# Kernel tuning notes

Hardware: AMD Instinct MI355X
Metric: run time of the kernel (lower is better)

## Reference

```python
import jax, jax.numpy as jnp
import numpy as np

N = 100000      # number of edge features (rows of feats)
M = 800000      # number of triplets
HID = 128
HEADS = 8
DH = HID // HEADS


def setup_inputs() -> dict:
    key = jax.random.key(0)
    ks = jax.random.split(key, 10)
    s = 1.0 / np.sqrt(HID)
    inp = {
        "feats": jax.random.normal(ks[0], (N, HID), dtype=jnp.float32),
        "idx_kj": jax.random.randint(ks[1], (M,), 0, N, dtype=jnp.int64),
        "idx_ji": jax.random.randint(ks[2], (M,), 0, N, dtype=jnp.int64),
        "Wv": jax.random.uniform(ks[3], (HID, HID), jnp.float32, -s, s),
        "Wq": jax.random.uniform(ks[4], (HID, HID), jnp.float32, -s, s),
        "Wk": jax.random.uniform(ks[5], (HID, HID), jnp.float32, -s, s),
        "W1": jax.random.uniform(ks[6], (HID, HID), jnp.float32, -s, s),
        "b1": jax.random.uniform(ks[7], (HID,), jnp.float32, -s, s),
        "W2": jax.random.uniform(ks[8], (HID, HID), jnp.float32, -s, s),
        "b2": jax.random.uniform(ks[9], (HID,), jnp.float32, -s, s),
    }
    return inp


def reference(feats, idx_kj, idx_ji, Wv, Wq, Wk, W1, b1, W2, b2):
    # Projections (no bias), reshape to [N, H, Dh]
    v = (feats @ Wv.T).reshape(N, HEADS, DH)
    k = (feats @ Wk.T).reshape(N, HEADS, DH)
    q = (feats @ Wq.T).reshape(N, HEADS, DH)

    # edge-indexed attention scores: [M, H, 1]
    att = jnp.sum(q[idx_kj] * k[idx_ji], axis=-1, keepdims=True)
    att = jnp.exp(jax.nn.leaky_relu(att, negative_slope=0.2))  # unsafe softmax, as in source

    # segment-sum normalizer over destination index idx_ji: [N, H, 1]
    denom = jax.ops.segment_sum(att, idx_ji, num_segments=N)
    att = att / denom[idx_ji]

    # weighted V gather-scatter: [M, HID] -> [N, HID]
    v_att = (v[idx_kj] * att).reshape(M, HID)
    agg = jax.ops.segment_sum(v_att, idx_ji, num_segments=N)  # v_clone after +scatter-v

    v_flat = v.reshape(N, HID)
    # ResidualLayer (dropout in eval mode -> identity): v + relu(lin2(relu(lin1(agg))))
    h = jax.nn.relu(agg @ W1.T + b1)
    h = jax.nn.relu(h @ W2.T + b2)
    return v_flat + h
```

## Files before the change

kernel.cpp:

```cpp
#include <hip/hip_runtime.h>
#include <hip/hip_bf16.h>
#include <math.h>

#define N_NODES 100000
#define M_EDGES 800000
#define HID 128
#define HEADS 8
#define DH 16
#define SCAN_NB ((N_NODES + 1023) / 1024)

typedef __attribute__((ext_vector_type(8))) short short8;
typedef __attribute__((ext_vector_type(4))) float floatx4;

__device__ __forceinline__ ushort f32_to_bf16(float x) {
    __hip_bfloat16 h = __float2bfloat16(x);
    union { __hip_bfloat16 h; ushort u; } c; c.h = h;
    return c.u;
}
__device__ __forceinline__ float bf16_bits_to_f32(ushort u) {
    union { unsigned int i; float f; } c; c.i = ((unsigned int)u) << 16;
    return c.f;
}
__device__ __forceinline__ float bf16pair_lo(unsigned int p) {
    union { unsigned int i; float f; } c; c.i = p << 16; return c.f;
}
__device__ __forceinline__ float bf16pair_hi(unsigned int p) {
    union { unsigned int i; float f; } c; c.i = p & 0xffff0000u; return c.f;
}

__device__ __forceinline__ void stage_w_frag(const ushort* __restrict__ W,
                                             ushort* __restrict__ lds, int tid)
{
    #pragma unroll
    for (int i = 0; i < 8; ++i) {
        int idx  = i * 256 + tid;
        int f    = idx >> 6;
        int lane = idx & 63;
        int t    = f & 7, ks = f >> 3;
        int row  = t * 16 + (lane & 15);
        int col  = ks * 32 + (lane >> 4) * 8;
        uint4 d = *(const uint4*)(W + row * HID + col);
        *(uint4*)(lds + idx * 8) = d;
    }
}

__global__ __launch_bounds__(256) void cvt_w_kernel(
    const float* __restrict__ Wq, const float* __restrict__ Wk, const float* __restrict__ Wv,
    const float* __restrict__ W1, const float* __restrict__ W2,
    ushort* __restrict__ dq, ushort* __restrict__ dk, ushort* __restrict__ dv,
    ushort* __restrict__ d1, ushort* __restrict__ d2)
{
    int i = blockIdx.x * 256 + threadIdx.x;
    int w = i >> 14;
    int j = i & 16383;
    const float* s[5] = {Wq, Wk, Wv, W1, W2};
    ushort*      d[5] = {dq, dk, dv, d1, d2};
    d[w][j] = f32_to_bf16(s[w][j]);
}

__global__ __launch_bounds__(256) void qkv_mfma_kernel(
    const float* __restrict__ feats,
    const ushort* __restrict__ Wq16, const ushort* __restrict__ Wk16, const ushort* __restrict__ Wv16,
    ushort* __restrict__ q16, ushort* __restrict__ k16, ushort* __restrict__ v16)
{
    __shared__ ushort wlds[16384];
    const int tid  = threadIdx.x;
    const int wave = tid >> 6;
    const int lane = tid & 63;
    const int row0 = blockIdx.x * 128 + wave * 32;
    const int lrow = lane & 15;
    const int lk   = (lane >> 4) * 8;
    const int crow = (lane >> 4) * 4;

    short8 afrag[2][4];
    bool tvalid[2];
    #pragma unroll
    for (int r = 0; r < 2; ++r) {
        int rr = row0 + r * 16;
        tvalid[r] = (rr < N_NODES);
        const float* arow = feats + (size_t)((tvalid[r] ? rr : 0) + lrow) * HID + lk;
        #pragma unroll
        for (int ks = 0; ks < 4; ++ks) {
            float4 f0 = *(const float4*)(arow + ks * 32);
            float4 f1 = *(const float4*)(arow + ks * 32 + 4);
            short8 a;
            a[0] = (short)f32_to_bf16(f0.x); a[1] = (short)f32_to_bf16(f0.y);
            a[2] = (short)f32_to_bf16(f0.z); a[3] = (short)f32_to_bf16(f0.w);
            a[4] = (short)f32_to_bf16(f1.x); a[5] = (short)f32_to_bf16(f1.y);
            a[6] = (short)f32_to_bf16(f1.z); a[7] = (short)f32_to_bf16(f1.w);
            afrag[r][ks] = a;
        }
    }

    const ushort* Ws[3] = {Wq16, Wk16, Wv16};
    ushort*       Os[3] = {q16, k16, v16};

    #pragma unroll
    for (int w = 0; w < 3; ++w) {
        __syncthreads();
        stage_w_frag(Ws[w], wlds, tid);
        __syncthreads();

        floatx4 acc[2][8];
        #pragma unroll
        for (int r = 0; r < 2; ++r)
            #pragma unroll
            for (int t = 0; t < 8; ++t) acc[r][t] = (floatx4)(0.f);

        #pragma unroll
        for (int ks = 0; ks < 4; ++ks) {
            short8 B[8];
            #pragma unroll
            for (int t = 0; t < 8; ++t)
                B[t] = *(const short8*)&wlds[(ks * 8 + t) * 512 + lane * 8];
            #pragma unroll
            for (int t = 0; t < 8; ++t) {
                acc[0][t] = __builtin_amdgcn_mfma_f32_16x16x32_bf16(B[t], afrag[0][ks], acc[0][t], 0, 0, 0);
                acc[1][t] = __builtin_amdgcn_mfma_f32_16x16x32_bf16(B[t], afrag[1][ks], acc[1][t], 0, 0, 0);
            }
        }

        #pragma unroll
        for (int r = 0; r < 2; ++r) {
            if (tvalid[r]) {
                ushort* O = Os[w] + (size_t)(row0 + r * 16 + lrow) * HID;
                #pragma unroll
                for (int t = 0; t < 8; ++t) {
                    ushort4 o;
                    o.x = f32_to_bf16(acc[r][t][0]); o.y = f32_to_bf16(acc[r][t][1]);
                    o.z = f32_to_bf16(acc[r][t][2]); o.w = f32_to_bf16(acc[r][t][3]);
                    *(ushort4*)(O + t * 16 + crow) = o;
                }
            }
        }
    }
}

__global__ __launch_bounds__(256) void hist_kernel(
    const int* __restrict__ idx_ji, int* __restrict__ count)
{
    int m = blockIdx.x * 256 + threadIdx.x;
    if (m < M_EDGES) atomicAdd(&count[idx_ji[m]], 1);
}

__global__ __launch_bounds__(256) void scan_blocksum_kernel(
    const int* __restrict__ count, int* __restrict__ blocksum)
{
    __shared__ int s[256];
    const int tid = threadIdx.x;
    const int base = blockIdx.x * 1024 + tid * 4;
    int sum = 0;
    if (base + 3 < N_NODES) {
        int4 c = *(const int4*)(count + base);
        sum = c.x + c.y + c.z + c.w;
    } else {
        #pragma unroll
        for (int j = 0; j < 4; ++j) if (base + j < N_NODES) sum += count[base + j];
    }
    s[tid] = sum;
    __syncthreads();
    for (int off = 128; off > 0; off >>= 1) {
        if (tid < off) s[tid] += s[tid + off];
        __syncthreads();
    }
    if (tid == 0) blocksum[blockIdx.x] = s[0];
}

__global__ __launch_bounds__(128) void scan_top_kernel(int* __restrict__ blocksum)
{
    __shared__ int s[128];
    const int t = threadIdx.x;
    int v = (t < SCAN_NB) ? blocksum[t] : 0;
    s[t] = v;
    __syncthreads();
    for (int off = 1; off < 128; off <<= 1) {
        int x = (t >= off) ? s[t - off] : 0;
        __syncthreads();
        s[t] += x;
        __syncthreads();
    }
    if (t < SCAN_NB) blocksum[t] = s[t] - v;
}

__global__ __launch_bounds__(256) void scan_write_kernel(
    const int* __restrict__ count, const int* __restrict__ blocksum,
    int* __restrict__ offsets, int* __restrict__ cursor)
{
    __shared__ int s[256];
    const int tid = threadIdx.x;
    const int base = blockIdx.x * 1024 + tid * 4;
    int c0 = 0, c1 = 0, c2 = 0, c3 = 0;
    if (base + 3 < N_NODES) {
        int4 c = *(const int4*)(count + base);
        c0 = c.x; c1 = c.y; c2 = c.z; c3 = c.w;
    } else {
        if (base     < N_NODES) c0 = count[base];
        if (base + 1 < N_NODES) c1 = count[base + 1];
        if (base + 2 < N_NODES) c2 = count[base + 2];
        if (base + 3 < N_NODES) c3 = count[base + 3];
    }
    const int tsum = c0 + c1 + c2 + c3;
    s[tid] = tsum;
    __syncthreads();
    for (int off = 1; off < 256; off <<= 1) {
        int x = (tid >= off) ? s[tid - off] : 0;
        __syncthreads();
        s[tid] += x;
        __syncthreads();
    }
    int o0 = s[tid] - tsum + blocksum[blockIdx.x];
    int o1 = o0 + c0, o2 = o1 + c1, o3 = o2 + c2;
    if (base + 3 < N_NODES) {
        *(int4*)(offsets + base) = make_int4(o0, o1, o2, o3);
        *(int4*)(cursor  + base) = make_int4(o0, o1, o2, o3);
    } else {
        if (base     < N_NODES) { offsets[base]     = o0; cursor[base]     = o0; }
        if (base + 1 < N_NODES) { offsets[base + 1] = o1; cursor[base + 1] = o1; }
        if (base + 2 < N_NODES) { offsets[base + 2] = o2; cursor[base + 2] = o2; }
        if (base + 3 < N_NODES) { offsets[base + 3] = o3; cursor[base + 3] = o3; }
    }
}

__global__ __launch_bounds__(256) void fill_kernel(
    const int* __restrict__ idx_ji, const int* __restrict__ idx_kj,
    int* __restrict__ cursor, int* __restrict__ edge_kj)
{
    int m = blockIdx.x * 256 + threadIdx.x;
    if (m < M_EDGES) {
        int pos = atomicAdd(&cursor[idx_ji[m]], 1);
        edge_kj[pos] = idx_kj[m];
    }
}

__global__ __launch_bounds__(256) void aggregate_kernel(
    const int* __restrict__ edge_kj, const int* __restrict__ offsets,
    const int* __restrict__ count, const ushort* __restrict__ q16,
    const ushort* __restrict__ k16, const ushort* __restrict__ v16,
    ushort* __restrict__ agg16)
{
    int gid  = blockIdx.x * 256 + threadIdx.x;
    int node = gid >> 6;
    int lane = threadIdx.x & 63;
    if (node >= N_NODES) return;

    const int deg  = count[node];
    const int base = offsets[node];

    unsigned int knp = *(const unsigned int*)(k16 + (size_t)node * HID + lane * 2);
    const float knx = bf16pair_lo(knp), kny = bf16pair_hi(knp);
    float accx = 0.f, accy = 0.f, d = 0.f;

    int e = 0;
    for (; e + 4 <= deg; e += 4) {
        int kj[4];
        #pragma unroll
        for (int i = 0; i < 4; ++i) kj[i] = edge_kj[base + e + i];
        unsigned int qp[4], vp[4];
        #pragma unroll
        for (int i = 0; i < 4; ++i) {
            qp[i] = *(const unsigned int*)(q16 + (size_t)kj[i] * HID + lane * 2);
            vp[i] = *(const unsigned int*)(v16 + (size_t)kj[i] * HID + lane * 2);
        }
        float p[4];
        #pragma unroll
        for (int i = 0; i < 4; ++i)
            p[i] = bf16pair_lo(qp[i]) * knx + bf16pair_hi(qp[i]) * kny;
        #pragma unroll
        for (int i = 0; i < 4; ++i) {
            p[i] += __shfl_xor(p[i], 1);
            p[i] += __shfl_xor(p[i], 2);
            p[i] += __shfl_xor(p[i], 4);
        }
        #pragma unroll
        for (int i = 0; i < 4; ++i) {
            float s = (p[i] >= 0.f) ? p[i] : 0.2f * p[i];
            s = expf(s);
            d += s;
            accx += s * bf16pair_lo(vp[i]);
            accy += s * bf16pair_hi(vp[i]);
        }
    }
    for (; e < deg; ++e) {
        int kj0 = edge_kj[base + e];
        unsigned int qp0 = *(const unsigned int*)(q16 + (size_t)kj0 * HID + lane * 2);
        unsigned int vp0 = *(const unsigned int*)(v16 + (size_t)kj0 * HID + lane * 2);
        float p0 = bf16pair_lo(qp0) * knx + bf16pair_hi(qp0) * kny;
        p0 += __shfl_xor(p0, 1); p0 += __shfl_xor(p0, 2); p0 += __shfl_xor(p0, 4);
        float s0 = (p0 >= 0.f) ? p0 : 0.2f * p0;
        s0 = expf(s0);
        d += s0;
        accx += s0 * bf16pair_lo(vp0);
        accy += s0 * bf16pair_hi(vp0);
    }

    const float inv = (deg > 0) ? 1.f / d : 0.f;
    unsigned int outp = (unsigned int)f32_to_bf16(accx * inv)
                      | ((unsigned int)f32_to_bf16(accy * inv) << 16);
    *(unsigned int*)(agg16 + (size_t)node * HID + lane * 2) = outp;
}

__global__ __launch_bounds__(256) void mlp_mfma_kernel(
    const ushort* __restrict__ agg16, const ushort* __restrict__ v16,
    const ushort* __restrict__ W1_16, const float* __restrict__ b1,
    const ushort* __restrict__ W2_16, const float* __restrict__ b2,
    float* __restrict__ out)
{
    __shared__ ushort wlds[16384];
    __shared__ ushort h1s[16384];
    const int tid  = threadIdx.x;
    const int wave = tid >> 6;
    const int lane = tid & 63;
    const int row0 = blockIdx.x * 128 + wave * 32;
    const int lrow = lane & 15;
    const int lk   = (lane >> 4) * 8;
    const int crow = (lane >> 4) * 4;

    short8 afrag[2][4];
    bool tvalid[2];
    #pragma unroll
    for (int r = 0; r < 2; ++r) {
        int rr = row0 + r * 16;
        tvalid[r] = (rr < N_NODES);
        const ushort* arow = agg16 + (size_t)((tvalid[r] ? rr : 0) + lrow) * HID + lk;
        #pragma unroll
        for (int ks = 0; ks < 4; ++ks)
            afrag[r][ks] = *(const short8*)(arow + ks * 32);
    }

    stage_w_frag(W1_16, wlds, tid);
    __syncthreads();

    {
        floatx4 acc[2][8];
        #pragma unroll
        for (int r = 0; r < 2; ++r)
            #pragma unroll
            for (int t = 0; t < 8; ++t) acc[r][t] = (floatx4)(0.f);
        #pragma unroll
        for (int ks = 0; ks < 4; ++ks) {
            short8 B[8];
            #pragma unroll
            for (int t = 0; t < 8; ++t)
                B[t] = *(const short8*)&wlds[(ks * 8 + t) * 512 + lane * 8];
            #pragma unroll
            for (int t = 0; t < 8; ++t) {
                acc[0][t] = __builtin_amdgcn_mfma_f32_16x16x32_bf16(B[t], afrag[0][ks], acc[0][t], 0, 0, 0);
                acc[1][t] = __builtin_amdgcn_mfma_f32_16x16x32_bf16(B[t], afrag[1][ks], acc[1][t], 0, 0, 0);
            }
        }
        #pragma unroll
        for (int r = 0; r < 2; ++r) {
            ushort* tile = &h1s[(wave * 2 + r) * 2048];
            #pragma unroll
            for (int t = 0; t < 8; ++t) {
                float4 bias = *(const float4*)(b1 + t * 16 + crow);
                ushort4 o;
                o.x = f32_to_bf16(fmaxf(acc[r][t][0] + bias.x, 0.f));
                o.y = f32_to_bf16(fmaxf(acc[r][t][1] + bias.y, 0.f));
                o.z = f32_to_bf16(fmaxf(acc[r][t][2] + bias.z, 0.f));
                o.w = f32_to_bf16(fmaxf(acc[r][t][3] + bias.w, 0.f));
                int ks   = t >> 1;
                int quad = (t & 1) * 2 + (crow >> 3);
                int j0   = crow & 4;
                *(ushort4*)(tile + (ks * 64 + quad * 16 + lrow) * 8 + j0) = o;
            }
        }
    }
    __syncthreads();
    stage_w_frag(W2_16, wlds, tid);
    __syncthreads();

    {
        short8 hfrag[2][4];
        #pragma unroll
        for (int r = 0; r < 2; ++r) {
            const ushort* tile = &h1s[(wave * 2 + r) * 2048];
            #pragma unroll
            for (int ks = 0; ks < 4; ++ks)
                hfrag[r][ks] = *(const short8*)(tile + (ks * 64 + lane) * 8);
        }
        floatx4 acc[2][8];
        #pragma unroll
        for (int r = 0; r < 2; ++r)
            #pragma unroll
            for (int t = 0; t < 8; ++t) acc[r][t] = (floatx4)(0.f);
        #pragma unroll
        for (int ks = 0; ks < 4; ++ks) {
            short8 B[8];
            #pragma unroll
            for (int t = 0; t < 8; ++t)
                B[t] = *(const short8*)&wlds[(ks * 8 + t) * 512 + lane * 8];
            #pragma unroll
            for (int t = 0; t < 8; ++t) {
                acc[0][t] = __builtin_amdgcn_mfma_f32_16x16x32_bf16(B[t], hfrag[0][ks], acc[0][t], 0, 0, 0);
                acc[1][t] = __builtin_amdgcn_mfma_f32_16x16x32_bf16(B[t], hfrag[1][ks], acc[1][t], 0, 0, 0);
            }
        }
        #pragma unroll
        for (int r = 0; r < 2; ++r) {
            if (tvalid[r]) {
                const size_t rowoff = (size_t)(row0 + r * 16 + lrow) * HID;
                #pragma unroll
                for (int t = 0; t < 8; ++t) {
                    float4 bias = *(const float4*)(b2 + t * 16 + crow);
                    ushort4 vv = *(const ushort4*)(v16 + rowoff + t * 16 + crow);
                    float4 o;
                    o.x = bf16_bits_to_f32(vv.x) + fmaxf(acc[r][t][0] + bias.x, 0.f);
                    o.y = bf16_bits_to_f32(vv.y) + fmaxf(acc[r][t][1] + bias.y, 0.f);
                    o.z = bf16_bits_to_f32(vv.z) + fmaxf(acc[r][t][2] + bias.z, 0.f);
                    o.w = bf16_bits_to_f32(vv.w) + fmaxf(acc[r][t][3] + bias.w, 0.f);
                    *(float4*)(out + rowoff + t * 16 + crow) = o;
                }
            }
        }
    }
}

extern "C" void kernel_launch(void* const* d_in, const int* in_sizes, int n_in,
                              void* d_out, int out_size, void* d_ws, size_t ws_size,
                              hipStream_t stream) {
    const float* feats  = (const float*)d_in[0];
    const int*   idx_kj = (const int*)d_in[1];
    const int*   idx_ji = (const int*)d_in[2];
    const float* Wv     = (const float*)d_in[3];
    const float* Wq     = (const float*)d_in[4];
    const float* Wk     = (const float*)d_in[5];
    const float* W1     = (const float*)d_in[6];
    const float* b1     = (const float*)d_in[7];
    const float* W2     = (const float*)d_in[8];
    const float* b2     = (const float*)d_in[9];
    float* out = (float*)d_out;

    ushort* q16     = (ushort*)d_ws;
    ushort* k16     = q16     + (size_t)N_NODES * HID;
    ushort* v16     = k16     + (size_t)N_NODES * HID;
    ushort* agg16   = v16     + (size_t)N_NODES * HID;
    ushort* Wq16    = agg16   + (size_t)N_NODES * HID;
    ushort* Wk16    = Wq16 + HID * HID;
    ushort* Wv16    = Wk16 + HID * HID;
    ushort* W116    = Wv16 + HID * HID;
    ushort* W216    = W116 + HID * HID;
    int* count      = (int*)(W216 + HID * HID);
    int* offsets    = count + N_NODES;
    int* cursor     = offsets + N_NODES;
    int* blocksum   = cursor + N_NODES;
    int* edge_kj    = blocksum + ((SCAN_NB + 3) & ~3);

    hipMemsetAsync(count, 0, N_NODES * sizeof(int), stream);

    cvt_w_kernel<<<(5 * HID * HID + 255) / 256, 256, 0, stream>>>(
        Wq, Wk, Wv, W1, W2, Wq16, Wk16, Wv16, W116, W216);

    qkv_mfma_kernel<<<(N_NODES + 127) / 128, 256, 0, stream>>>(
        feats, Wq16, Wk16, Wv16, q16, k16, v16);

    hist_kernel<<<(M_EDGES + 255) / 256, 256, 0, stream>>>(idx_ji, count);
    scan_blocksum_kernel<<<SCAN_NB, 256, 0, stream>>>(count, blocksum);
    scan_top_kernel<<<1, 128, 0, stream>>>(blocksum);
    scan_write_kernel<<<SCAN_NB, 256, 0, stream>>>(count, blocksum, offsets, cursor);
    fill_kernel<<<(M_EDGES + 255) / 256, 256, 0, stream>>>(idx_ji, idx_kj, cursor, edge_kj);

    aggregate_kernel<<<(N_NODES * 64 + 255) / 256, 256, 0, stream>>>(
        edge_kj, offsets, count, q16, k16, v16, agg16);

    mlp_mfma_kernel<<<(N_NODES + 127) / 128, 256, 0, stream>>>(
        agg16, v16, W116, b1, W216, b2, out);
}
```

Measured before the change: 329.6 us.

## Interleave Q and V rows and aggregate with 16 lanes per node

The Q and V projections are now written into one interleaved buffer (256 bf16 per node), so each edge gather pulls Q and V from adjacent memory. The aggregate kernel now gives each node 16 lanes instead of 64, with each lane loading 16-byte vectors (8 channels). This cuts the shuffle reduction to one step, and the kernel also switches to the fast __expf. The aim is fewer, wider memory transactions and more nodes per wave in the gather-heavy aggregation. In exchange, each lane holds more registers and the edge loop is unrolled by 2 instead of 4, which may reduce memory-level parallelism.

```diff
diff --git a/kernel.cpp b/kernel.cpp
--- a/kernel.cpp
+++ b/kernel.cpp
@@ -61,7 +61,7 @@
 __global__ __launch_bounds__(256) void qkv_mfma_kernel(
     const float* __restrict__ feats,
     const ushort* __restrict__ Wq16, const ushort* __restrict__ Wk16, const ushort* __restrict__ Wv16,
-    ushort* __restrict__ q16, ushort* __restrict__ k16, ushort* __restrict__ v16)
+    ushort* __restrict__ qv16, ushort* __restrict__ k16)
 {
     __shared__ ushort wlds[16384];
     const int tid  = threadIdx.x;
@@ -93,7 +93,10 @@
     }
 
     const ushort* Ws[3] = {Wq16, Wk16, Wv16};
-    ushort*       Os[3] = {q16, k16, v16};
+    ushort* Ob[3]; int Ostride[3];
+    Ob[0] = qv16;       Ostride[0] = 256;
+    Ob[1] = k16;        Ostride[1] = 128;
+    Ob[2] = qv16 + 128; Ostride[2] = 256;
 
     #pragma unroll
     for (int w = 0; w < 3; ++w) {
@@ -123,7 +126,7 @@
         #pragma unroll
         for (int r = 0; r < 2; ++r) {
             if (tvalid[r]) {
-                ushort* O = Os[w] + (size_t)(row0 + r * 16 + lrow) * HID;
+                ushort* O = Ob[w] + (size_t)(row0 + r * 16 + lrow) * Ostride[w];
                 #pragma unroll
                 for (int t = 0; t < 8; ++t) {
                     ushort4 o;
@@ -234,73 +237,99 @@
 
 __global__ __launch_bounds__(256) void aggregate_kernel(
     const int* __restrict__ edge_kj, const int* __restrict__ offsets,
-    const int* __restrict__ count, const ushort* __restrict__ q16,
-    const ushort* __restrict__ k16, const ushort* __restrict__ v16,
-    ushort* __restrict__ agg16)
-{
-    int gid  = blockIdx.x * 256 + threadIdx.x;
-    int node = gid >> 6;
-    int lane = threadIdx.x & 63;
+    const int* __restrict__ count, const ushort* __restrict__ qv16,
+    const ushort* __restrict__ k16, ushort* __restrict__ agg16)
+{
+    const int gid  = blockIdx.x * 256 + threadIdx.x;
+    const int node = gid >> 4;
+    const int l16  = threadIdx.x & 15;
     if (node >= N_NODES) return;
 
     const int deg  = count[node];
     const int base = offsets[node];
 
-    unsigned int knp = *(const unsigned int*)(k16 + (size_t)node * HID + lane * 2);
-    const float knx = bf16pair_lo(knp), kny = bf16pair_hi(knp);
-    float accx = 0.f, accy = 0.f, d = 0.f;
+    float kn[8];
+    {
+        uint4 kp = *(const uint4*)(k16 + (size_t)node * HID + l16 * 8);
+        const unsigned int* kw = (const unsigned int*)&kp;
+        #pragma unroll
+        for (int j = 0; j < 4; ++j) {
+            kn[2*j]   = bf16pair_lo(kw[j]);
+            kn[2*j+1] = bf16pair_hi(kw[j]);
+        }
+    }
+
+    float acc[8] = {0.f,0.f,0.f,0.f,0.f,0.f,0.f,0.f};
+    float d = 0.f;
 
     int e = 0;
-    for (; e + 4 <= deg; e += 4) {
-        int kj[4];
-        #pragma unroll
-        for (int i = 0; i < 4; ++i) kj[i] = edge_kj[base + e + i];
-        unsigned int qp[4], vp[4];
-        #pragma unroll
-        for (int i = 0; i < 4; ++i) {
-            qp[i] = *(const unsigned int*)(q16 + (size_t)kj[i] * HID + lane * 2);
-            vp[i] = *(const unsigned int*)(v16 + (size_t)kj[i] * HID + lane * 2);
-        }
-        float p[4];
-        #pragma unroll
-        for (int i = 0; i < 4; ++i)
-            p[i] = bf16pair_lo(qp[i]) * knx + bf16pair_hi(qp[i]) * kny;
-        #pragma unroll
-        for (int i = 0; i < 4; ++i) {
-            p[i] += __shfl_xor(p[i], 1);
-            p[i] += __shfl_xor(p[i], 2);
-            p[i] += __shfl_xor(p[i], 4);
-        }
-        #pragma unroll
-        for (int i = 0; i < 4; ++i) {
-            float s = (p[i] >= 0.f) ? p[i] : 0.2f * p[i];
-            s = expf(s);
-            d += s;
-            accx += s * bf16pair_lo(vp[i]);
-            accy += s * bf16pair_hi(vp[i]);
-        }
-    }
-    for (; e < deg; ++e) {
-        int kj0 = edge_kj[base + e];
-        unsigned int qp0 = *(const unsigned int*)(q16 + (size_t)kj0 * HID + lane * 2);
-        unsigned int vp0 = *(const unsigned int*)(v16 + (size_t)kj0 * HID + lane * 2);
-        float p0 = bf16pair_lo(qp0) * knx + bf16pair_hi(qp0) * kny;
-        p0 += __shfl_xor(p0, 1); p0 += __shfl_xor(p0, 2); p0 += __shfl_xor(p0, 4);
-        float s0 = (p0 >= 0.f) ? p0 : 0.2f * p0;
-        s0 = expf(s0);
+    for (; e + 2 <= deg; e += 2) {
+        const int kj0 = edge_kj[base + e];
+        const int kj1 = edge_kj[base + e + 1];
+        const ushort* r0 = qv16 + (size_t)kj0 * 256 + l16 * 8;
+        const ushort* r1 = qv16 + (size_t)kj1 * 256 + l16 * 8;
+        uint4 qp0 = *(const uint4*)r0;
+        uint4 vp0 = *(const uint4*)(r0 + 128);
+        uint4 qp1 = *(const uint4*)r1;
+        uint4 vp1 = *(const uint4*)(r1 + 128);
+
+        const unsigned int* q0 = (const unsigned int*)&qp0;
+        const unsigned int* q1 = (const unsigned int*)&qp1;
+        float p0 = 0.f, p1 = 0.f;
+        #pragma unroll
+        for (int j = 0; j < 4; ++j) {
+            p0 += bf16pair_lo(q0[j]) * kn[2*j] + bf16pair_hi(q0[j]) * kn[2*j+1];
+            p1 += bf16pair_lo(q1[j]) * kn[2*j] + bf16pair_hi(q1[j]) * kn[2*j+1];
+        }
+        p0 += __shfl_xor(p0, 1);
+        p1 += __shfl_xor(p1, 1);
+        float lr0 = (p0 >= 0.f) ? p0 : 0.2f * p0;
+        float lr1 = (p1 >= 0.f) ? p1 : 0.2f * p1;
+        float s0 = __expf(lr0);
+        float s1 = __expf(lr1);
+        d += s0 + s1;
+        const unsigned int* v0 = (const unsigned int*)&vp0;
+        const unsigned int* v1 = (const unsigned int*)&vp1;
+        #pragma unroll
+        for (int j = 0; j < 4; ++j) {
+            acc[2*j]   += s0 * bf16pair_lo(v0[j]) + s1 * bf16pair_lo(v1[j]);
+            acc[2*j+1] += s0 * bf16pair_hi(v0[j]) + s1 * bf16pair_hi(v1[j]);
+        }
+    }
+    if (e < deg) {
+        const int kj0 = edge_kj[base + e];
+        const ushort* r0 = qv16 + (size_t)kj0 * 256 + l16 * 8;
+        uint4 qp0 = *(const uint4*)r0;
+        uint4 vp0 = *(const uint4*)(r0 + 128);
+        const unsigned int* q0 = (const unsigned int*)&qp0;
+        float p0 = 0.f;
+        #pragma unroll
+        for (int j = 0; j < 4; ++j)
+            p0 += bf16pair_lo(q0[j]) * kn[2*j] + bf16pair_hi(q0[j]) * kn[2*j+1];
+        p0 += __shfl_xor(p0, 1);
+        float lr0 = (p0 >= 0.f) ? p0 : 0.2f * p0;
+        float s0 = __expf(lr0);
         d += s0;
-        accx += s0 * bf16pair_lo(vp0);
-        accy += s0 * bf16pair_hi(vp0);
+        const unsigned int* v0 = (const unsigned int*)&vp0;
+        #pragma unroll
+        for (int j = 0; j < 4; ++j) {
+            acc[2*j]   += s0 * bf16pair_lo(v0[j]);
+            acc[2*j+1] += s0 * bf16pair_hi(v0[j]);
+        }
     }
 
     const float inv = (deg > 0) ? 1.f / d : 0.f;
-    unsigned int outp = (unsigned int)f32_to_bf16(accx * inv)
-                      | ((unsigned int)f32_to_bf16(accy * inv) << 16);
-    *(unsigned int*)(agg16 + (size_t)node * HID + lane * 2) = outp;
+    uint4 o;
+    unsigned int* ow = (unsigned int*)&o;
+    #pragma unroll
+    for (int j = 0; j < 4; ++j)
+        ow[j] = (unsigned int)f32_to_bf16(acc[2*j] * inv)
+              | ((unsigned int)f32_to_bf16(acc[2*j+1] * inv) << 16);
+    *(uint4*)(agg16 + (size_t)node * HID + l16 * 8) = o;
 }
 
 __global__ __launch_bounds__(256) void mlp_mfma_kernel(
-    const ushort* __restrict__ agg16, const ushort* __restrict__ v16,
+    const ushort* __restrict__ agg16, const ushort* __restrict__ qv16,
     const ushort* __restrict__ W1_16, const float* __restrict__ b1,
     const ushort* __restrict__ W2_16, const float* __restrict__ b2,
     float* __restrict__ out)
@@ -399,17 +428,19 @@
         #pragma unroll
         for (int r = 0; r < 2; ++r) {
             if (tvalid[r]) {
-                const size_t rowoff = (size_t)(row0 + r * 16 + lrow) * HID;
+                const size_t nrow = (size_t)(row0 + r * 16 + lrow);
+                const ushort* vrow = qv16 + nrow * 256 + 128;
+                float* orow = out + nrow * HID;
                 #pragma unroll
                 for (int t = 0; t < 8; ++t) {
                     float4 bias = *(const float4*)(b2 + t * 16 + crow);
-                    ushort4 vv = *(const ushort4*)(v16 + rowoff + t * 16 + crow);
+                    ushort4 vv = *(const ushort4*)(vrow + t * 16 + crow);
                     float4 o;
                     o.x = bf16_bits_to_f32(vv.x) + fmaxf(acc[r][t][0] + bias.x, 0.f);
                     o.y = bf16_bits_to_f32(vv.y) + fmaxf(acc[r][t][1] + bias.y, 0.f);
                     o.z = bf16_bits_to_f32(vv.z) + fmaxf(acc[r][t][2] + bias.z, 0.f);
                     o.w = bf16_bits_to_f32(vv.w) + fmaxf(acc[r][t][3] + bias.w, 0.f);
-                    *(float4*)(out + rowoff + t * 16 + crow) = o;
+                    *(float4*)(orow + t * 16 + crow) = o;
                 }
             }
         }
@@ -431,10 +462,9 @@
     const float* b2     = (const float*)d_in[9];
     float* out = (float*)d_out;
 
-    ushort* q16     = (ushort*)d_ws;
-    ushort* k16     = q16     + (size_t)N_NODES * HID;
-    ushort* v16     = k16     + (size_t)N_NODES * HID;
-    ushort* agg16   = v16     + (size_t)N_NODES * HID;
+    ushort* qv16    = (ushort*)d_ws;
+    ushort* k16     = qv16    + (size_t)N_NODES * 256;
+    ushort* agg16   = k16     + (size_t)N_NODES * HID;
     ushort* Wq16    = agg16   + (size_t)N_NODES * HID;
     ushort* Wk16    = Wq16 + HID * HID;
     ushort* Wv16    = Wk16 + HID * HID;
@@ -452,7 +482,7 @@
         Wq, Wk, Wv, W1, W2, Wq16, Wk16, Wv16, W116, W216);
 
     qkv_mfma_kernel<<<(N_NODES + 127) / 128, 256, 0, stream>>>(
-        feats, Wq16, Wk16, Wv16, q16, k16, v16);
+        feats, Wq16, Wk16, Wv16, qv16, k16);
 
     hist_kernel<<<(M_EDGES + 255) / 256, 256, 0, stream>>>(idx_ji, count);
     scan_blocksum_kernel<<<SCAN_NB, 256, 0, stream>>>(count, blocksum);
@@ -460,9 +490,9 @@
     scan_write_kernel<<<SCAN_NB, 256, 0, stream>>>(count, blocksum, offsets, cursor);
     fill_kernel<<<(M_EDGES + 255) / 256, 256, 0, stream>>>(idx_ji, idx_kj, cursor, edge_kj);
 
-    aggregate_kernel<<<(N_NODES * 64 + 255) / 256, 256, 0, stream>>>(
-        edge_kj, offsets, count, q16, k16, v16, agg16);
+    aggregate_kernel<<<((size_t)N_NODES * 16 + 255) / 256, 256, 0, stream>>>(
+        edge_kj, offsets, count, qv16, k16, agg16);
 
     mlp_mfma_kernel<<<(N_NODES + 127) / 128, 256, 0, stream>>>(
-        agg16, v16, W116, b1, W216, b2, out);
-}
+        agg16, qv16, W116, b1, W216, b2, out);
+}
```

After: 328.5 us. Within noise of the previous version (-0.3%).
